# Kernel tuning notes

Measured on AMD Instinct MI355X. Metric: run time of the kernel, lower is better.

Reference implementation:

```python
import math
import jax, jax.numpy as jnp
import numpy as np

N = 256          # num_spins
DIM = 64         # vector dimension of each spin
BETA = 1.0
MAX_ITER = 40    # solver_fwd_max_iter
TOL = 1e-4       # solver_fwd_tol
J_STD = 1.0 / np.sqrt(N * DIM * 2)


def _J_eff(J_raw):
    # symmetrize + traceless, as in VectorSpinModel.J()
    J = 0.5 * (J_raw + J_raw.T)
    return J * (1.0 - jnp.eye(N, dtype=J.dtype))


def _V_and_inv(t, J):
    # t: (b, 1) -> expand to (b, N); V = diag_embed(t) - J
    b = t.shape[0]
    tfull = jnp.broadcast_to(t, (b, N))
    V = jnp.eye(N, dtype=t.dtype) * tfull[:, :, None] - J[None]  # (b, N, N)
    I = jnp.broadcast_to(jnp.eye(N, dtype=t.dtype), V.shape)
    V_inv = jnp.linalg.solve(V, I)
    return tfull, V, V_inv


def _grad_t_phi(t, h, J, beta):
    # scalar-t branch: t has shape (b, 1)
    _, _, V_inv = _V_and_inv(t, J)
    tr = jnp.trace(V_inv, axis1=-2, axis2=-1)                     # (b,)
    y = V_inv @ h                                                  # (b, N, f)
    z = V_inv @ y                                                  # V_inv @ V_inv @ h
    quad = jnp.sum(h * z, axis=(-2, -1))                           # h^T Vinv Vinv h
    g = beta * N - 0.5 * tr - beta / (4.0 * DIM) * quad            # (b,)
    return g[:, None]


def _newton(t0, h, J, beta):
    def g(t):
        return _grad_t_phi(t, h, J, beta)

    def step(t, _):
        f, df = jax.jvp(g, (t,), (jnp.ones_like(t),))
        upd = jnp.where(jnp.abs(f) > TOL, f / df, jnp.zeros_like(f))
        return t - upd, None

    t_star, _ = jax.lax.scan(step, t0, None, length=MAX_ITER)
    return t_star


def _phi(t, h, J, beta):
    tfull, V, V_inv = _V_and_inv(t, J)
    _, logabsdet = jnp.linalg.slogdet(V)
    quad = jnp.sum(h * (V_inv @ h), axis=(-2, -1))  # einsum bif,bij,bjf->b
    return beta * tfull.sum(-1) - 0.5 * logabsdet + beta / (4.0 * DIM) * quad


def setup_inputs() -> dict:
    key = jax.random.key(0)
    k1, k2 = jax.random.split(key)
    x = jax.random.normal(k1, (64, N, DIM), dtype=jnp.float32)
    J_raw = jax.random.normal(k2, (N, N), dtype=jnp.float32) * J_STD
    return {"x": x, "J_raw": J_raw}


def reference(x, J_raw):
    J = _J_eff(J_raw)
    h = x  # _prepare_sources is identity
    t0 = jnp.ones((x.shape[0], 1), dtype=x.dtype)
    t_star = _newton(t0, h, J, BETA)
    phi = _phi(t_star, h, J, BETA)
    afe = -(1.0 / BETA) * (0.5 * jnp.log(jnp.asarray(math.pi / BETA, x.dtype)) + phi / N)
    return afe, jax.lax.stop_gradient(t_star)
```

## Files before the change

kernel.cpp:

```cpp
#include <hip/hip_runtime.h>
#include <math.h>

#define NN 256
#define DIMF 64
#define BATCH 64
#define PB 4
#define NB (BATCH + PB)
#define KMAX 12
#define NM (KMAX + 1)
#define NSTEPS (KMAX / 2)
#define CG 2
#define CW 32
#define YSTR 264

using short8 = __attribute__((ext_vector_type(8))) short;
using f32x4  = __attribute__((ext_vector_type(4))) float;

__device__ __forceinline__ float bf2f(unsigned short u) {
    union { unsigned int i; float f; } v; v.i = ((unsigned int)u) << 16; return v.f;
}
__device__ __forceinline__ unsigned short f2bf(float f) {
    union { float f; unsigned int i; } v; v.f = f;
    unsigned int b = v.i;
    return (unsigned short)((b + 0x7FFFu + ((b >> 16) & 1u)) >> 16);
}

__global__ void jbuild_kernel(const float* __restrict__ Jr,
                              unsigned short* __restrict__ Jb,
                              float* __restrict__ m) {
    int i = blockIdx.x * 256 + threadIdx.x;
    int r = i >> 8, c = i & 255;
    float v = (r == c) ? 0.0f : 0.5f * (Jr[i] + Jr[(c << 8) + r]);
    Jb[i] = f2bf(v);
    if (i < NB * NM) m[i] = 0.0f;
}

__global__ __launch_bounds__(256)
void chain_kernel(const unsigned short* __restrict__ J,
                  const float* __restrict__ x,
                  float* __restrict__ m) {
    __shared__ unsigned short ybuf[2][CW][YSTR];
    const int g = blockIdx.x;
    const int b = blockIdx.y;
    const int t = threadIdx.x;
    const int w = t >> 6;
    const int lane = t & 63;
    const int quad = lane >> 4;
    const int l15 = lane & 15;
    const int n0 = g * CW;

    if (b < BATCH) {
        const float* xb = x + (b << 14) + n0;
        float s0 = 0.f;
        #pragma unroll
        for (int it = 0; it < 8; ++it) {
            int k = it * 32 + (t >> 3);
            int nn = (t & 7) * 4;
            const float4 v = *(const float4*)(xb + (k << 6) + nn);
            s0 += v.x * v.x + v.y * v.y + v.z * v.z + v.w * v.w;
            ybuf[0][nn + 0][k] = f2bf(v.x);
            ybuf[0][nn + 1][k] = f2bf(v.y);
            ybuf[0][nn + 2][k] = f2bf(v.z);
            ybuf[0][nn + 3][k] = f2bf(v.w);
        }
        #pragma unroll
        for (int o = 32; o > 0; o >>= 1) s0 += __shfl_down(s0, o);
        if (lane == 0) atomicAdd(&m[b * NM], s0);
    } else {
        int p = b - BATCH;
        for (int i = t; i < CW * 256; i += 256) ybuf[0][i >> 8][i & 255] = 0;
        __syncthreads();
        if (t < CW) ybuf[0][t][p * 64 + n0 + t] = 0x3F80;
    }
    __syncthreads();

    int cur = 0;
    for (int j = 1; j <= NSTEPS; ++j) {
        f32x4 acc[4][2] = {};
        #pragma unroll
        for (int kc = 0; kc < 8; ++kc) {
            const int kb = kc * 32 + quad * 8;
            short8 bfrag[2];
            #pragma unroll
            for (int nt = 0; nt < 2; ++nt)
                bfrag[nt] = *(const short8*)&ybuf[cur][nt * 16 + l15][kb];
            #pragma unroll
            for (int mt = 0; mt < 4; ++mt) {
                short8 afrag = *(const short8*)(J + ((w * 64 + mt * 16 + l15) << 8) + kb);
                #pragma unroll
                for (int nt = 0; nt < 2; ++nt)
                    acc[mt][nt] = __builtin_amdgcn_mfma_f32_16x16x32_bf16(
                        afrag, bfrag[nt], acc[mt][nt], 0, 0, 0);
            }
        }

        const int nxt = cur ^ 1;
        float d1 = 0.f, d2 = 0.f;
        #pragma unroll
        for (int mt = 0; mt < 4; ++mt) {
            int mbase = w * 64 + mt * 16 + quad * 4;
            #pragma unroll
            for (int nt = 0; nt < 2; ++nt) {
                int col = nt * 16 + l15;
                #pragma unroll
                for (int r = 0; r < 4; ++r) {
                    float v = acc[mt][nt][r];
                    int row = mbase + r;
                    d1 += bf2f(ybuf[cur][col][row]) * v;
                    d2 += v * v;
                    ybuf[nxt][col][row] = f2bf(v);
                }
            }
        }
        #pragma unroll
        for (int o = 32; o > 0; o >>= 1) {
            d1 += __shfl_down(d1, o);
            d2 += __shfl_down(d2, o);
        }
        if (lane == 0) {
            atomicAdd(&m[b * NM + 2 * j - 1], d1);
            atomicAdd(&m[b * NM + 2 * j],     d2);
        }
        cur = nxt;
        __syncthreads();
    }
}

__global__ void solve_kernel(const float* __restrict__ m, float* __restrict__ out) {
    int b = threadIdx.x;
    if (b >= BATCH) return;
    float mk[NM], Tk[NM];
    mk[0] = m[b * NM];
    Tk[0] = 256.0f;
    for (int k = 1; k < NM; ++k) {
        mk[k] = m[b * NM + k];
        float s = 0.f;
        for (int p = 0; p < PB; ++p) s += m[(BATCH + p) * NM + k];
        Tk[k] = s;
    }
    float t = 1.0f;
    for (int it = 0; it < 40; ++it) {
        float inv = 1.0f / t;
        float p1 = inv, S1 = 0.f, S1d = 0.f, S3 = 0.f, S3d = 0.f;
        for (int k = 0; k < NM; ++k) {
            float p2 = p1 * inv;
            float p3 = p2 * inv;
            float kp1 = (float)(k + 1);
            S1  += Tk[k] * p1;
            S1d += kp1 * Tk[k] * p2;
            S3  += kp1 * mk[k] * p2;
            S3d += kp1 * (float)(k + 2) * mk[k] * p3;
            p1 = p2;
        }
        float f  = 256.0f - 0.5f * S1 - S3 * (1.0f / 256.0f);
        float df = 0.5f * S1d + S3d * (1.0f / 256.0f);
        if (fabsf(f) <= 1e-4f) break;
        t -= f / df;
    }
    float inv = 1.0f / t;
    float logdet = 256.0f * logf(t);
    float quad = 0.f;
    float p1 = inv, pk = 1.0f;
    for (int k = 0; k < NM; ++k) {
        quad += mk[k] * p1;
        if (k >= 1) { pk *= inv; logdet -= Tk[k] / (float)k * pk; }
        p1 *= inv;
    }
    float phi = 256.0f * t - 0.5f * logdet + quad * (1.0f / 256.0f);
    float afe = -(0.5f * logf((float)M_PI) + phi * (1.0f / 256.0f));
    out[b] = afe;
    out[BATCH + b] = t;
}

extern "C" void kernel_launch(void* const* d_in, const int* in_sizes, int n_in,
                              void* d_out, int out_size, void* d_ws, size_t ws_size,
                              hipStream_t stream) {
    const float* x  = (const float*)d_in[0];
    const float* Jr = (const float*)d_in[1];
    float* out = (float*)d_out;

    char* base = (char*)d_ws;
    unsigned short* Jb = (unsigned short*)base;
    float* m = (float*)(base + 131072);

    jbuild_kernel<<<256, 256, 0, stream>>>(Jr, Jb, m);
    chain_kernel<<<dim3(CG, NB), 256, 0, stream>>>(Jb, x, m);
    solve_kernel<<<1, 64, 0, stream>>>(m, out);
}
```

Measured before the change: 72.24 us.

## Hold J fragments in registers, split columns across more blocks with 512 threads

The chain kernel now uses 4 column groups of 16 and 512 threads per block, so each of the 8 waves owns 32 rows of J. J is stored in a k-chunked layout so each wave can load its A fragments into registers once, before the iteration loop, instead of re-reading them from global memory every step. The epilogue uses vectorized 4-element LDS reads and writes and skips the final unneeded write. This doubles the block count and raises register pressure through the 16 short8 J fragments held per thread.

```diff
diff --git a/kernel.cpp b/kernel.cpp
--- a/kernel.cpp
+++ b/kernel.cpp
@@ -9,12 +9,13 @@
 #define KMAX 12
 #define NM (KMAX + 1)
 #define NSTEPS (KMAX / 2)
-#define CG 2
-#define CW 32
+#define CG 4
+#define CW 16
 #define YSTR 264
 
-using short8 = __attribute__((ext_vector_type(8))) short;
-using f32x4  = __attribute__((ext_vector_type(4))) float;
+using short4v = __attribute__((ext_vector_type(4))) short;
+using short8  = __attribute__((ext_vector_type(8))) short;
+using f32x4   = __attribute__((ext_vector_type(4))) float;
 
 __device__ __forceinline__ float bf2f(unsigned short u) {
     union { unsigned int i; float f; } v; v.i = ((unsigned int)u) << 16; return v.f;
@@ -31,15 +32,15 @@
     int i = blockIdx.x * 256 + threadIdx.x;
     int r = i >> 8, c = i & 255;
     float v = (r == c) ? 0.0f : 0.5f * (Jr[i] + Jr[(c << 8) + r]);
-    Jb[i] = f2bf(v);
+    Jb[((c >> 3) << 11) + (r << 3) + (c & 7)] = f2bf(v);
     if (i < NB * NM) m[i] = 0.0f;
 }
 
-__global__ __launch_bounds__(256)
+__global__ __launch_bounds__(512, 4)
 void chain_kernel(const unsigned short* __restrict__ J,
                   const float* __restrict__ x,
                   float* __restrict__ m) {
-    __shared__ unsigned short ybuf[2][CW][YSTR];
+    __shared__ __align__(16) unsigned short ybuf[2][CW][YSTR];
     const int g = blockIdx.x;
     const int b = blockIdx.y;
     const int t = threadIdx.x;
@@ -47,15 +48,24 @@
     const int lane = t & 63;
     const int quad = lane >> 4;
     const int l15 = lane & 15;
-    const int n0 = g * CW;
+
+    short8 jreg[2][8];
+    #pragma unroll
+    for (int mt = 0; mt < 2; ++mt) {
+        const int row = w * 32 + mt * 16 + l15;
+        #pragma unroll
+        for (int kc = 0; kc < 8; ++kc)
+            jreg[mt][kc] = *(const short8*)(J + ((((kc << 2) | quad) << 11) + (row << 3)));
+    }
 
     if (b < BATCH) {
-        const float* xb = x + (b << 14) + n0;
+        const float* xb = x + (b << 14) + (g << 4);
         float s0 = 0.f;
         #pragma unroll
-        for (int it = 0; it < 8; ++it) {
-            int k = it * 32 + (t >> 3);
-            int nn = (t & 7) * 4;
+        for (int it = 0; it < 2; ++it) {
+            const int idx = it * 512 + t;
+            const int k = idx >> 2;
+            const int nn = (idx & 3) << 2;
             const float4 v = *(const float4*)(xb + (k << 6) + nn);
             s0 += v.x * v.x + v.y * v.y + v.z * v.z + v.w * v.w;
             ybuf[0][nn + 0][k] = f2bf(v.x);
@@ -67,50 +77,41 @@
         for (int o = 32; o > 0; o >>= 1) s0 += __shfl_down(s0, o);
         if (lane == 0) atomicAdd(&m[b * NM], s0);
     } else {
-        int p = b - BATCH;
-        for (int i = t; i < CW * 256; i += 256) ybuf[0][i >> 8][i & 255] = 0;
-        __syncthreads();
-        if (t < CW) ybuf[0][t][p * 64 + n0 + t] = 0x3F80;
+        const int p = b - BATCH;
+        #pragma unroll
+        for (int i = t; i < CW * 256; i += 512) {
+            const int c = i >> 8, k = i & 255;
+            ybuf[0][c][k] = (k == p * 64 + g * 16 + c) ? 0x3F80 : 0;
+        }
     }
     __syncthreads();
 
     int cur = 0;
     for (int j = 1; j <= NSTEPS; ++j) {
-        f32x4 acc[4][2] = {};
+        f32x4 acc0 = {}, acc1 = {};
         #pragma unroll
         for (int kc = 0; kc < 8; ++kc) {
             const int kb = kc * 32 + quad * 8;
-            short8 bfrag[2];
-            #pragma unroll
-            for (int nt = 0; nt < 2; ++nt)
-                bfrag[nt] = *(const short8*)&ybuf[cur][nt * 16 + l15][kb];
-            #pragma unroll
-            for (int mt = 0; mt < 4; ++mt) {
-                short8 afrag = *(const short8*)(J + ((w * 64 + mt * 16 + l15) << 8) + kb);
-                #pragma unroll
-                for (int nt = 0; nt < 2; ++nt)
-                    acc[mt][nt] = __builtin_amdgcn_mfma_f32_16x16x32_bf16(
-                        afrag, bfrag[nt], acc[mt][nt], 0, 0, 0);
-            }
+            const short8 bfrag = *(const short8*)&ybuf[cur][l15][kb];
+            acc0 = __builtin_amdgcn_mfma_f32_16x16x32_bf16(jreg[0][kc], bfrag, acc0, 0, 0, 0);
+            acc1 = __builtin_amdgcn_mfma_f32_16x16x32_bf16(jreg[1][kc], bfrag, acc1, 0, 0, 0);
         }
 
         const int nxt = cur ^ 1;
         float d1 = 0.f, d2 = 0.f;
         #pragma unroll
-        for (int mt = 0; mt < 4; ++mt) {
-            int mbase = w * 64 + mt * 16 + quad * 4;
+        for (int mt = 0; mt < 2; ++mt) {
+            const int rb = w * 32 + mt * 16 + quad * 4;
+            const short4v yp = *(const short4v*)&ybuf[cur][l15][rb];
+            short4v yn;
             #pragma unroll
-            for (int nt = 0; nt < 2; ++nt) {
-                int col = nt * 16 + l15;
-                #pragma unroll
-                for (int r = 0; r < 4; ++r) {
-                    float v = acc[mt][nt][r];
-                    int row = mbase + r;
-                    d1 += bf2f(ybuf[cur][col][row]) * v;
-                    d2 += v * v;
-                    ybuf[nxt][col][row] = f2bf(v);
-                }
+            for (int r = 0; r < 4; ++r) {
+                const float v = (mt == 0) ? acc0[r] : acc1[r];
+                d1 += bf2f((unsigned short)yp[r]) * v;
+                d2 += v * v;
+                yn[r] = (short)f2bf(v);
             }
+            if (j < NSTEPS) *(short4v*)&ybuf[nxt][l15][rb] = yn;
         }
         #pragma unroll
         for (int o = 32; o > 0; o >>= 1) {
@@ -184,6 +185,6 @@
     float* m = (float*)(base + 131072);
 
     jbuild_kernel<<<256, 256, 0, stream>>>(Jr, Jb, m);
-    chain_kernel<<<dim3(CG, NB), 256, 0, stream>>>(Jb, x, m);
+    chain_kernel<<<dim3(CG, NB), 512, 0, stream>>>(Jb, x, m);
     solve_kernel<<<1, 64, 0, stream>>>(m, out);
 }
```

After: 74.21 us. +2.7%, slower.
